# Performance work log

Hardware: AMD Instinct MI355X
Metric: run time of the kernel (lower is better)

The kernel has to match this reference:

```python
import jax, jax.numpy as jnp
import numpy as np

N, E = 50000, 800000
DIN, DH, DOUT = 128, 128, 64


def setup_inputs() -> dict:
    key = jax.random.key(0)
    k = jax.random.split(key, 6)
    node_features = jax.random.normal(k[0], (N, DIN), dtype=jnp.float32)
    edge_src = jax.random.randint(k[1], (E,), 0, N)
    edge_dst = jax.random.randint(k[2], (E,), 0, N)
    # Glorot-ish init for the two GCNConv weight matrices, zero bias (PyG default bias=True)
    W1 = jax.random.normal(k[3], (DIN, DH), dtype=jnp.float32) * (1.0 / np.sqrt(DIN))
    b1 = jnp.zeros((DH,), dtype=jnp.float32)
    W2 = jax.random.normal(k[4], (DH, DOUT), dtype=jnp.float32) * (1.0 / np.sqrt(DH))
    b2 = jnp.zeros((DOUT,), dtype=jnp.float32)
    return {"node_features": node_features, "edge_src": edge_src, "edge_dst": edge_dst,
            "W1": W1, "b1": b1, "W2": W2, "b2": b2}


def gcn_conv(x, W, b, src, dst, n):
    """PyG GCNConv: add self-loops, symmetric D^-1/2 (A+I) D^-1/2 normalization."""
    xw = x @ W  # [n, d_out]
    loops = jnp.arange(n, dtype=src.dtype)
    s = jnp.concatenate([src, loops])  # edges + self-loops
    d = jnp.concatenate([dst, loops])
    deg = jax.ops.segment_sum(jnp.ones_like(d, dtype=xw.dtype), d, num_segments=n)
    dinv = jnp.where(deg > 0, jax.lax.rsqrt(deg), 0.0)
    norm = dinv[s] * dinv[d]  # [E + n]
    msg = xw[s] * norm[:, None]  # gather + scale (memory-bound)
    out = jax.ops.segment_sum(msg, d, num_segments=n)  # scatter-add
    return out + b


def reference(node_features, edge_src, edge_dst, W1, b1, W2, b2):
    n = node_features.shape[0]
    h = gcn_conv(node_features, W1, b1, edge_src, edge_dst, n)
    h = jax.nn.relu(h)  # dropout omitted (inference / eval mode)
    h = gcn_conv(h, W2, b2, edge_src, edge_dst, n)
    # EdgePredictor: per-edge dot product of endpoint representations
    score = jnp.sum(h[edge_src] * h[edge_dst], axis=-1)  # [E]
    return score
```

## Files before the change

### kernel.cpp

```cpp
#include <hip/hip_runtime.h>
#include <hip/hip_bf16.h>
#include <type_traits>


#define DIN 128
#define DH  128
#define DOUT 64
#define CAP 8192

typedef __attribute__((ext_vector_type(8))) short short8;
typedef __attribute__((ext_vector_type(4))) float floatx4;

__device__ inline float2 bf2_to_f2(unsigned u) {
    union { unsigned i; float f; } a, b;
    a.i = u << 16;
    b.i = u & 0xffff0000u;
    return make_float2(a.f, b.f);
}
__device__ inline float bf_to_f(unsigned short u) {
    union { unsigned i; float f; } a;
    a.i = ((unsigned)u) << 16;
    return a.f;
}
__device__ inline unsigned short f_to_bf(float f) {
    union { float f; unsigned i; } v; v.f = f;
    unsigned r = v.i + 0x7fffu + ((v.i >> 16) & 1u);
    return (unsigned short)(r >> 16);
}

__global__ __launch_bounds__(256) void bucket_count_kernel(const int* __restrict__ dst,
                                                           int* __restrict__ gcnt,
                                                           int E, int nbuck) {
    __shared__ int hist[256];
    int t = threadIdx.x;
    hist[t] = 0;
    __syncthreads();
    int base = blockIdx.x * 4096 + t;
#pragma unroll
    for (int it = 0; it < 16; ++it) {
        int e = base + it * 256;
        if (e < E) atomicAdd(&hist[dst[e] >> 8], 1);
    }
    __syncthreads();
    if (t < nbuck && hist[t]) atomicAdd(&gcnt[t], hist[t]);
}

__global__ __launch_bounds__(256) void scan_buckets_kernel(const int* __restrict__ gcnt,
                                                           int* __restrict__ gbase,
                                                           int* __restrict__ gcursor,
                                                           int* __restrict__ row_ptr,
                                                           int nbuck, int N, int E) {
    __shared__ int lds[256];
    int t = threadIdx.x;
    int v = (t < nbuck) ? gcnt[t] : 0;
    lds[t] = v;
    __syncthreads();
    for (int off = 1; off < 256; off <<= 1) {
        int u = (t >= off) ? lds[t - off] : 0;
        __syncthreads();
        lds[t] += u;
        __syncthreads();
    }
    int ex = lds[t] - v;
    if (t < nbuck) { gbase[t] = ex; gcursor[t] = ex; }
    if (t == 0) { gbase[nbuck] = E; row_ptr[N] = E; }
}

__global__ __launch_bounds__(256) void bucket_place_kernel(const int* __restrict__ src,
                                                           const int* __restrict__ dst,
                                                           int* __restrict__ gcursor,
                                                           uint2* __restrict__ tmp,
                                                           int E, int nbuck) {
    __shared__ int hist[256];
    __shared__ int cur[256];
    int t = threadIdx.x;
    hist[t] = 0;
    __syncthreads();
    int base = blockIdx.x * 4096 + t;
    int d[16];
#pragma unroll
    for (int it = 0; it < 16; ++it) {
        int e = base + it * 256;
        d[it] = (e < E) ? dst[e] : -1;
        if (d[it] >= 0) atomicAdd(&hist[d[it] >> 8], 1);
    }
    __syncthreads();
    if (t < nbuck && hist[t]) cur[t] = atomicAdd(&gcursor[t], hist[t]);
    __syncthreads();
#pragma unroll
    for (int it = 0; it < 16; ++it) {
        int e = base + it * 256;
        if (d[it] >= 0) {
            int r = atomicAdd(&cur[d[it] >> 8], 1);
            tmp[r] = make_uint2((unsigned)src[e], (unsigned)d[it]);
        }
    }
}

__global__ __launch_bounds__(256) void bucket_csr_kernel(const uint2* __restrict__ tmp,
                                                         const int* __restrict__ gbase,
                                                         int* __restrict__ row_ptr,
                                                         float* __restrict__ dinv,
                                                         int* __restrict__ col, int N) {
    __shared__ int hist[256], cur[256], pfx[256];
    __shared__ unsigned esrc[CAP];
    __shared__ unsigned char eloc[CAP];
    __shared__ unsigned sorted[CAP];
    int b = blockIdx.x, t = threadIdx.x;
    int beg = gbase[b], end = gbase[b + 1];
    int size = end - beg;
    if (size > CAP) size = CAP;
    hist[t] = 0;
    __syncthreads();
    for (int i = t; i < size; i += 256) {
        uint2 e = tmp[beg + i];
        esrc[i] = e.x;
        int loc = e.y & 255;
        eloc[i] = (unsigned char)loc;
        atomicAdd(&hist[loc], 1);
    }
    __syncthreads();
    int v = hist[t];
    pfx[t] = v;
    __syncthreads();
    for (int off = 1; off < 256; off <<= 1) {
        int u = (t >= off) ? pfx[t - off] : 0;
        __syncthreads();
        pfx[t] += u;
        __syncthreads();
    }
    int ex = pfx[t] - v;
    cur[t] = ex;
    int node = b * 256 + t;
    if (node < N) {
        row_ptr[node] = beg + ex;
        dinv[node] = rsqrtf((float)(v + 1));
    }
    __syncthreads();
    for (int i = t; i < size; i += 256) {
        int r = atomicAdd(&cur[eloc[i]], 1);
        sorted[r] = esrc[i];
    }
    __syncthreads();
    for (int i = t; i < size; i += 256) col[beg + i] = (int)sorted[i];
}

template <int COLS, typename XT>
__global__ __launch_bounds__(256) void mfma_gemm_kernel(const XT* __restrict__ X,
                                                        const float* __restrict__ W,
                                                        const float* __restrict__ dinv,
                                                        unsigned short* __restrict__ Y,
                                                        int nrows) {
    constexpr int KP = 136;
    __shared__ unsigned short Xs[128 * KP];
    __shared__ unsigned short Wt[COLS * KP];
    int tid = threadIdx.x;
    int row0 = blockIdx.x * 128;

    if constexpr (std::is_same_v<XT, float>) {
#pragma unroll
        for (int it = 0; it < 16; ++it) {
            int idx = it * 256 + tid;
            int r = idx >> 5;
            int c4 = (idx & 31) * 4;
            int gr = row0 + r; if (gr >= nrows) gr = nrows - 1;
            float4 v = *(const float4*)(X + (size_t)gr * 128 + c4);
            ushort4 p;
            p.x = f_to_bf(v.x); p.y = f_to_bf(v.y);
            p.z = f_to_bf(v.z); p.w = f_to_bf(v.w);
            *(ushort4*)&Xs[r * KP + c4] = p;
        }
    } else {
#pragma unroll
        for (int it = 0; it < 8; ++it) {
            int idx = it * 256 + tid;
            int r = idx >> 4;
            int c8 = (idx & 15) * 8;
            int gr = row0 + r; if (gr >= nrows) gr = nrows - 1;
            uint4 v = *(const uint4*)(X + (size_t)gr * 128 + c8);
            *(uint4*)&Xs[r * KP + c8] = v;
        }
    }
#pragma unroll
    for (int it = 0; it < COLS / 8; ++it) {
        int idx = it * 256 + tid;
        int n = idx >> 5;
        int k4 = (idx & 31) * 4;
        ushort4 p;
        p.x = f_to_bf(W[(size_t)(k4 + 0) * COLS + n]);
        p.y = f_to_bf(W[(size_t)(k4 + 1) * COLS + n]);
        p.z = f_to_bf(W[(size_t)(k4 + 2) * COLS + n]);
        p.w = f_to_bf(W[(size_t)(k4 + 3) * COLS + n]);
        *(ushort4*)&Wt[n * KP + k4] = p;
    }
    __syncthreads();

    constexpr int CT = COLS / 16;
    int wv = tid >> 6, lane = tid & 63;
    int lr = lane & 15;
    int lk = (lane >> 4) * 8;
    int rw = wv * 32;

    floatx4 acc[2][CT];
#pragma unroll
    for (int rt = 0; rt < 2; ++rt)
#pragma unroll
        for (int ct = 0; ct < CT; ++ct) acc[rt][ct] = (floatx4){0.f, 0.f, 0.f, 0.f};

#pragma unroll
    for (int kk = 0; kk < 128; kk += 32) {
        short8 a[2], b[CT];
#pragma unroll
        for (int rt = 0; rt < 2; ++rt)
            a[rt] = *(const short8*)&Xs[(rw + rt * 16 + lr) * KP + kk + lk];
#pragma unroll
        for (int ct = 0; ct < CT; ++ct)
            b[ct] = *(const short8*)&Wt[(ct * 16 + lr) * KP + kk + lk];
#pragma unroll
        for (int rt = 0; rt < 2; ++rt)
#pragma unroll
            for (int ct = 0; ct < CT; ++ct)
                acc[rt][ct] = __builtin_amdgcn_mfma_f32_16x16x32_bf16(
                    a[rt], b[ct], acc[rt][ct], 0, 0, 0);
    }

#pragma unroll
    for (int rt = 0; rt < 2; ++rt) {
#pragma unroll
        for (int i = 0; i < 4; ++i) {
            int grow = row0 + rw + rt * 16 + (lane >> 4) * 4 + i;
            if (grow >= nrows) continue;
            float dv = dinv[grow];
#pragma unroll
            for (int ct = 0; ct < CT; ++ct)
                Y[(size_t)grow * COLS + ct * 16 + lr] =
                    f_to_bf(acc[rt][ct][i] * dv);
        }
    }
}

template <int D, bool RELU>
__global__ __launch_bounds__(256) void agg_kernel(const unsigned short* __restrict__ y,
                                                  const int* __restrict__ row_ptr,
                                                  const int* __restrict__ col,
                                                  const float* __restrict__ dinv,
                                                  const float* __restrict__ bias,
                                                  unsigned short* __restrict__ out, int n) {
    constexpr int V = D / 64;
    int w = (blockIdx.x * 256 + threadIdx.x) >> 6;
    int lane = threadIdx.x & 63;
    if (w >= n) return;
    float acc[V];
    if constexpr (V == 2) {
        float2 t = bf2_to_f2(*(const unsigned*)(y + (size_t)w * D + lane * 2));
        acc[0] = t.x; acc[1] = t.y;
    } else {
        acc[0] = bf_to_f(y[(size_t)w * D + lane]);
    }
    int beg = row_ptr[w], end = row_ptr[w + 1];
    int i = beg;
    for (; i + 8 <= end; i += 8) {
        int s[8];
#pragma unroll
        for (int u = 0; u < 8; ++u) s[u] = col[i + u];
        if constexpr (V == 2) {
            unsigned tv[8];
#pragma unroll
            for (int u = 0; u < 8; ++u)
                tv[u] = *(const unsigned*)(y + (size_t)s[u] * D + lane * 2);
#pragma unroll
            for (int u = 0; u < 8; ++u) {
                float2 f = bf2_to_f2(tv[u]);
                acc[0] += f.x; acc[1] += f.y;
            }
        } else {
            unsigned short tv[8];
#pragma unroll
            for (int u = 0; u < 8; ++u) tv[u] = y[(size_t)s[u] * D + lane];
#pragma unroll
            for (int u = 0; u < 8; ++u) acc[0] += bf_to_f(tv[u]);
        }
    }
    for (; i < end; ++i) {
        int s = col[i];
        if constexpr (V == 2) {
            float2 f = bf2_to_f2(*(const unsigned*)(y + (size_t)s * D + lane * 2));
            acc[0] += f.x; acc[1] += f.y;
        } else {
            acc[0] += bf_to_f(y[(size_t)s * D + lane]);
        }
    }
    float dv = dinv[w];
    if constexpr (V == 2) {
        float r0 = fmaf(dv, acc[0], bias[lane * 2]);
        float r1 = fmaf(dv, acc[1], bias[lane * 2 + 1]);
        if (RELU) { r0 = fmaxf(r0, 0.f); r1 = fmaxf(r1, 0.f); }
        unsigned pk = (unsigned)f_to_bf(r0) | ((unsigned)f_to_bf(r1) << 16);
        *(unsigned*)(out + (size_t)w * D + lane * 2) = pk;
    } else {
        float r = fmaf(dv, acc[0], bias[lane]);
        if (RELU) r = fmaxf(r, 0.f);
        out[(size_t)w * D + lane] = f_to_bf(r);
    }
}

__global__ __launch_bounds__(256) void score_kernel(const unsigned short* __restrict__ h2,
                                                    const int* __restrict__ src,
                                                    const int* __restrict__ dst,
                                                    float* __restrict__ out, int E) {
    int tid = blockIdx.x * 256 + threadIdx.x;
    int e = tid >> 4;
    if (e >= E) return;
    int q = tid & 15;
    int s = src[e], d = dst[e];
    uint2 ua = *(const uint2*)(h2 + (size_t)s * 64 + q * 4);
    uint2 ub = *(const uint2*)(h2 + (size_t)d * 64 + q * 4);
    float2 a0 = bf2_to_f2(ua.x), a1 = bf2_to_f2(ua.y);
    float2 b0 = bf2_to_f2(ub.x), b1 = bf2_to_f2(ub.y);
    float v = a0.x * b0.x + a0.y * b0.y + a1.x * b1.x + a1.y * b1.y;
    v += __shfl_xor(v, 8);
    v += __shfl_xor(v, 4);
    v += __shfl_xor(v, 2);
    v += __shfl_xor(v, 1);
    if (q == 0) out[e] = v;
}

extern "C" void kernel_launch(void* const* d_in, const int* in_sizes, int n_in,
                              void* d_out, int out_size, void* d_ws, size_t ws_size,
                              hipStream_t stream) {
    const float* X   = (const float*)d_in[0];
    const int*   src = (const int*)d_in[1];
    const int*   dst = (const int*)d_in[2];
    const float* W1  = (const float*)d_in[3];
    const float* b1  = (const float*)d_in[4];
    const float* W2  = (const float*)d_in[5];
    const float* b2  = (const float*)d_in[6];
    float* score = (float*)d_out;

    const int N = in_sizes[0] / DIN;
    const int E = in_sizes[1];
    const int nbuck = (N + 255) / 256;
    const int EB = (E + 4095) / 4096;

    auto align = [](size_t x) { return (x + 255) & ~(size_t)255; };
    char* p = (char*)d_ws;
    int*   gcnt    = (int*)p;               p += align(256 * 4);
    int*   gbase   = (int*)p;               p += align(257 * 4);
    int*   gcursor = (int*)p;               p += align(256 * 4);
    int*   row_ptr = (int*)p;               p += align((size_t)(N + 1) * 4);
    float* dinv    = (float*)p;             p += align((size_t)N * 4);
    int*   col     = (int*)p;               p += align((size_t)E * 4);
    uint2* tmp     = (uint2*)p;             p += align((size_t)E * 8);
    unsigned short* y1 = (unsigned short*)p; p += align((size_t)N * DH * 2);
    unsigned short* h1 = (unsigned short*)p; p += align((size_t)N * DH * 2);
    unsigned short* y2 = y1;
    unsigned short* h2 = y1 + (size_t)N * DOUT;

    hipMemsetAsync(gcnt, 0, 256 * 4, stream);

    bucket_count_kernel<<<EB, 256, 0, stream>>>(dst, gcnt, E, nbuck);
    scan_buckets_kernel<<<1, 256, 0, stream>>>(gcnt, gbase, gcursor, row_ptr, nbuck, N, E);
    bucket_place_kernel<<<EB, 256, 0, stream>>>(src, dst, gcursor, tmp, E, nbuck);
    bucket_csr_kernel<<<nbuck, 256, 0, stream>>>(tmp, gbase, row_ptr, dinv, col, N);

    int gemm_blocks = (N + 127) / 128;
    mfma_gemm_kernel<DH, float><<<gemm_blocks, 256, 0, stream>>>(X, W1, dinv, y1, N);

    int agg_blocks = (N + 3) / 4;
    agg_kernel<DH, true><<<agg_blocks, 256, 0, stream>>>(y1, row_ptr, col, dinv, b1, h1, N);

    mfma_gemm_kernel<DOUT, unsigned short><<<gemm_blocks, 256, 0, stream>>>(h1, W2, dinv, y2, N);
    agg_kernel<DOUT, false><<<agg_blocks, 256, 0, stream>>>(y2, row_ptr, col, dinv, b2, h2, N);

    int score_blocks = (E * 16 + 255) / 256;
    score_kernel<<<score_blocks, 256, 0, stream>>>(h2, src, dst, score, E);
}
```

Baseline: 261.1 us.

## Compute edge scores in CSR order, reusing destination rows and scattering by edge index

The edge-score pass now runs per destination node over the CSR built for aggregation. Each node's h2 row is loaded once into registers, and only the source rows are gathered per edge. To write scores back in the original edge order, the CSR build now also records the original edge index, packing the source id and local destination slot into one 32-bit word. The cost is an extra E-sized index array, more shared memory in the CSR kernel, scattered 4-byte output writes, and a source id limited to 16 bits.

```diff
diff --git a/kernel.cpp b/kernel.cpp
--- a/kernel.cpp
+++ b/kernel.cpp
@@ -92,7 +92,8 @@
         int e = base + it * 256;
         if (d[it] >= 0) {
             int r = atomicAdd(&cur[d[it] >> 8], 1);
-            tmp[r] = make_uint2((unsigned)src[e], (unsigned)d[it]);
+            tmp[r] = make_uint2((unsigned)src[e] | ((unsigned)(d[it] & 255) << 16),
+                                (unsigned)e);
         }
     }
 }
@@ -101,11 +102,13 @@
                                                          const int* __restrict__ gbase,
                                                          int* __restrict__ row_ptr,
                                                          float* __restrict__ dinv,
-                                                         int* __restrict__ col, int N) {
+                                                         int* __restrict__ col,
+                                                         int* __restrict__ eidx, int N) {
     __shared__ int hist[256], cur[256], pfx[256];
-    __shared__ unsigned esrc[CAP];
-    __shared__ unsigned char eloc[CAP];
-    __shared__ unsigned sorted[CAP];
+    __shared__ unsigned ebuf[CAP];
+    __shared__ unsigned ibuf[CAP];
+    __shared__ unsigned ssrc[CAP];
+    __shared__ unsigned sidx[CAP];
     int b = blockIdx.x, t = threadIdx.x;
     int beg = gbase[b], end = gbase[b + 1];
     int size = end - beg;
@@ -114,10 +117,9 @@
     __syncthreads();
     for (int i = t; i < size; i += 256) {
         uint2 e = tmp[beg + i];
-        esrc[i] = e.x;
-        int loc = e.y & 255;
-        eloc[i] = (unsigned char)loc;
-        atomicAdd(&hist[loc], 1);
+        ebuf[i] = e.x;
+        ibuf[i] = e.y;
+        atomicAdd(&hist[e.x >> 16], 1);
     }
     __syncthreads();
     int v = hist[t];
@@ -138,11 +140,15 @@
     }
     __syncthreads();
     for (int i = t; i < size; i += 256) {
-        int r = atomicAdd(&cur[eloc[i]], 1);
-        sorted[r] = esrc[i];
-    }
-    __syncthreads();
-    for (int i = t; i < size; i += 256) col[beg + i] = (int)sorted[i];
+        int r = atomicAdd(&cur[ebuf[i] >> 16], 1);
+        ssrc[r] = ebuf[i] & 0xffffu;
+        sidx[r] = ibuf[i];
+    }
+    __syncthreads();
+    for (int i = t; i < size; i += 256) {
+        col[beg + i]  = (int)ssrc[i];
+        eidx[beg + i] = (int)sidx[i];
+    }
 }
 
 template <int COLS, typename XT>
@@ -304,25 +310,40 @@
     }
 }
 
-__global__ __launch_bounds__(256) void score_kernel(const unsigned short* __restrict__ h2,
-                                                    const int* __restrict__ src,
-                                                    const int* __restrict__ dst,
-                                                    float* __restrict__ out, int E) {
-    int tid = blockIdx.x * 256 + threadIdx.x;
-    int e = tid >> 4;
-    if (e >= E) return;
-    int q = tid & 15;
-    int s = src[e], d = dst[e];
-    uint2 ua = *(const uint2*)(h2 + (size_t)s * 64 + q * 4);
-    uint2 ub = *(const uint2*)(h2 + (size_t)d * 64 + q * 4);
-    float2 a0 = bf2_to_f2(ua.x), a1 = bf2_to_f2(ua.y);
-    float2 b0 = bf2_to_f2(ub.x), b1 = bf2_to_f2(ub.y);
-    float v = a0.x * b0.x + a0.y * b0.y + a1.x * b1.x + a1.y * b1.y;
-    v += __shfl_xor(v, 8);
-    v += __shfl_xor(v, 4);
-    v += __shfl_xor(v, 2);
-    v += __shfl_xor(v, 1);
-    if (q == 0) out[e] = v;
+__global__ __launch_bounds__(256) void score_csr_kernel(const unsigned short* __restrict__ h2,
+                                                        const int* __restrict__ row_ptr,
+                                                        const int* __restrict__ col,
+                                                        const int* __restrict__ eidx,
+                                                        float* __restrict__ out, int n) {
+    int w = (blockIdx.x * 256 + threadIdx.x) >> 6;
+    int lane = threadIdx.x & 63;
+    if (w >= n) return;
+    int q = lane & 7;
+    uint4 hd = *(const uint4*)(h2 + (size_t)w * 64 + q * 8);
+    float d0[8];
+    { float2 f;
+      f = bf2_to_f2(hd.x); d0[0] = f.x; d0[1] = f.y;
+      f = bf2_to_f2(hd.y); d0[2] = f.x; d0[3] = f.y;
+      f = bf2_to_f2(hd.z); d0[4] = f.x; d0[5] = f.y;
+      f = bf2_to_f2(hd.w); d0[6] = f.x; d0[7] = f.y; }
+    int beg = row_ptr[w], end = row_ptr[w + 1];
+    int g = lane >> 3;
+    for (int i = beg; i < end; i += 8) {
+        int ei = i + g;
+        bool ok = ei < end;
+        int s = ok ? col[ei] : 0;
+        uint4 hs = *(const uint4*)(h2 + (size_t)s * 64 + q * 8);
+        float v = 0.f;
+        float2 f;
+        f = bf2_to_f2(hs.x); v = fmaf(d0[0], f.x, v); v = fmaf(d0[1], f.y, v);
+        f = bf2_to_f2(hs.y); v = fmaf(d0[2], f.x, v); v = fmaf(d0[3], f.y, v);
+        f = bf2_to_f2(hs.z); v = fmaf(d0[4], f.x, v); v = fmaf(d0[5], f.y, v);
+        f = bf2_to_f2(hs.w); v = fmaf(d0[6], f.x, v); v = fmaf(d0[7], f.y, v);
+        v += __shfl_xor(v, 4);
+        v += __shfl_xor(v, 2);
+        v += __shfl_xor(v, 1);
+        if (ok && q == 0) out[eidx[ei]] = v;
+    }
 }
 
 extern "C" void kernel_launch(void* const* d_in, const int* in_sizes, int n_in,
@@ -350,6 +371,7 @@
     int*   row_ptr = (int*)p;               p += align((size_t)(N + 1) * 4);
     float* dinv    = (float*)p;             p += align((size_t)N * 4);
     int*   col     = (int*)p;               p += align((size_t)E * 4);
+    int*   eidx    = (int*)p;               p += align((size_t)E * 4);
     uint2* tmp     = (uint2*)p;             p += align((size_t)E * 8);
     unsigned short* y1 = (unsigned short*)p; p += align((size_t)N * DH * 2);
     unsigned short* h1 = (unsigned short*)p; p += align((size_t)N * DH * 2);
@@ -361,7 +383,7 @@
     bucket_count_kernel<<<EB, 256, 0, stream>>>(dst, gcnt, E, nbuck);
     scan_buckets_kernel<<<1, 256, 0, stream>>>(gcnt, gbase, gcursor, row_ptr, nbuck, N, E);
     bucket_place_kernel<<<EB, 256, 0, stream>>>(src, dst, gcursor, tmp, E, nbuck);
-    bucket_csr_kernel<<<nbuck, 256, 0, stream>>>(tmp, gbase, row_ptr, dinv, col, N);
+    bucket_csr_kernel<<<nbuck, 256, 0, stream>>>(tmp, gbase, row_ptr, dinv, col, eidx, N);
 
     int gemm_blocks = (N + 127) / 128;
     mfma_gemm_kernel<DH, float><<<gemm_blocks, 256, 0, stream>>>(X, W1, dinv, y1, N);
@@ -372,6 +394,5 @@
     mfma_gemm_kernel<DOUT, unsigned short><<<gemm_blocks, 256, 0, stream>>>(h1, W2, dinv, y2, N);
     agg_kernel<DOUT, false><<<agg_blocks, 256, 0, stream>>>(y2, row_ptr, col, dinv, b2, h2, N);
 
-    int score_blocks = (E * 16 + 255) / 256;
-    score_kernel<<<score_blocks, 256, 0, stream>>>(h2, src, dst, score, E);
-}
+    score_csr_kernel<<<agg_blocks, 256, 0, stream>>>(h2, row_ptr, col, eidx, score, N);
+}
```

New measurement: 255.9 us. -2.0%, faster.
